# Performance work log

Measured on AMD Instinct MI355X. Metric: run time of the kernel, lower is better.

The kernel has to match this reference:

```python
import jax, jax.numpy as jnp
import numpy as np

B, C, H, W = 32, 16, 256, 256
NUM_BINS = 9
LEVELS = 3
EPS = 1e-8

def _dw_kernels():
    lap = np.array([[0, 1, 0], [1, -4, 1], [0, 1, 0]], np.float32)
    sx = np.array([[-1, 0, 1], [-2, 0, 2], [-1, 0, 1]], np.float32)
    sy = np.array([[-1, -2, -1], [0, 0, 0], [1, 2, 1]], np.float32)
    rep = lambda k: np.tile(k[None, None], (C, 1, 1, 1))  # [C,1,3,3] depthwise
    return rep(lap), rep(sx), rep(sy)

def setup_inputs() -> dict:
    key = jax.random.key(0)
    x = jax.random.normal(key, (B, C, H, W), dtype=jnp.float32)
    lap_k, sx_k, sy_k = _dw_kernels()
    return {"x": x, "lap_k": jnp.asarray(lap_k), "sx_k": jnp.asarray(sx_k), "sy_k": jnp.asarray(sy_k)}

def _dwconv(x, k):
    # depthwise 3x3, padding=1, groups=C
    return jax.lax.conv_general_dilated(
        x, k, window_strides=(1, 1), padding=[(1, 1), (1, 1)],
        dimension_numbers=("NCHW", "OIHW", "NCHW"), feature_group_count=C)

def reference(x, lap_k, sx_k, sy_k):
    lap = _dwconv(x, lap_k)
    gx = _dwconv(lap, sx_k)
    gy = _dwconv(lap, sy_k)
    mag = jnp.sqrt(gx * gx + gy * gy + EPS)
    ang = jnp.mod(jnp.arctan2(gy, gx) * (180.0 / np.pi), 180.0)
    bin_size = 180.0 / NUM_BINS
    bins = jnp.floor((ang + 0.5 * bin_size) / bin_size).astype(jnp.int32) % NUM_BINS

    BC = B * C
    mag_bc = mag.reshape(BC, H * W)
    bins_bc = bins.reshape(BC, H * W)
    row_ids = jnp.arange(BC)[:, None]

    hists = []
    for lvl in range(LEVELS):
        cs = 2 ** lvl
        cell_h, cell_w = H // cs, W // cs
        Wc = W // cell_w
        rows = jnp.arange(H) // cell_h
        cols = jnp.arange(W) // cell_w
        cell_id = (rows[:, None] * Wc + cols[None, :]).reshape(-1)  # [H*W]
        num_cells = cs * cs
        idx = cell_id[None, :] * NUM_BINS + bins_bc  # [BC, H*W]
        hist = jnp.zeros((BC, num_cells * NUM_BINS), mag.dtype).at[row_ids, idx].add(mag_bc)
        hist = hist.reshape(BC, num_cells, NUM_BINS)
        hist = hist / (hist.sum(axis=-1, keepdims=True) + EPS)          # L1-ish norm
        norm = jnp.sqrt(jnp.sum(hist * hist, axis=-1, keepdims=True))
        hist = hist / jnp.maximum(norm, 1e-12)                          # F.normalize p=2
        hists.append(hist.reshape(B, C * num_cells, NUM_BINS))
    out = jnp.concatenate(hists, axis=1)[:, None]  # [B,1,C*(1+4+16),num_bins]
    return out
```

## Files before the change

kernel.cpp:

```cpp
#include <hip/hip_runtime.h>


#define H_IMG 256
#define W_IMG 256

__device__ __forceinline__ void lap_row6(float dst[6], const float u[8], const float m[8],
                                         const float d[8], float wm0, float wm5, float rowm) {
#pragma unroll
  for (int c = 0; c < 6; ++c) {
    float v = (u[c + 1] + d[c + 1]) + fmaf(-4.f, m[c + 1], m[c] + m[c + 2]);
    dst[c] = v * rowm;
  }
  dst[0] *= wm0;
  dst[5] *= wm5;
}

__device__ __forceinline__ void out_row4(const float A[6], const float B[6], const float C[6],
                                         float acc[10]) {
  float cs[6], dd[6];
#pragma unroll
  for (int c = 0; c < 6; ++c) {
    cs[c] = A[c] + fmaf(2.f, B[c], C[c]);
    dd[c] = C[c] - A[c];
  }
#pragma unroll
  for (int c = 0; c < 4; ++c) {
    float gx = cs[c + 2] - cs[c];
    float gy = fmaf(2.f, dd[c + 1], dd[c] + dd[c + 2]);
    float mag = __builtin_amdgcn_sqrtf(fmaf(gx, gx, fmaf(gy, gy, 1e-8f)));
    bool neg = gy < 0.f;
    float fx = neg ? -gx : gx;
    float fy = neg ? -gy : gy;
    float u, v;
    u = 0.17364817766693033f * fx; v = 0.984807753012208f * fy;
    acc[0] += (u <= v) ? mag : 0.f;
    acc[8] += (u <= -v) ? mag : 0.f;
    u = 0.5f * fx; v = 0.8660254037844387f * fy;
    acc[1] += (u <= v) ? mag : 0.f;
    acc[7] += (u <= -v) ? mag : 0.f;
    u = 0.766044443118978f * fx; v = 0.6427876096865393f * fy;
    acc[2] += (u <= v) ? mag : 0.f;
    acc[6] += (u <= -v) ? mag : 0.f;
    u = 0.9396926207859084f * fx; v = 0.3420201433256687f * fy;
    acc[3] += (u <= v) ? mag : 0.f;
    acc[5] += (u <= -v) ? mag : 0.f;
    acc[4] += (fx <= 0.f) ? mag : 0.f;
    acc[9] += mag;
  }
}

__device__ __forceinline__ void load_grow(const float* __restrict__ xim, int gr, bool valid,
                                          int o0, int o1, int o2, int o3,
                                          float mlo, float mhi, float r[8]) {
  if (valid) {
    const float* p = xim + gr * W_IMG;
    float2 a = *reinterpret_cast<const float2*>(p + o0);
    float2 b = *reinterpret_cast<const float2*>(p + o1);
    float2 c = *reinterpret_cast<const float2*>(p + o2);
    float2 d = *reinterpret_cast<const float2*>(p + o3);
    r[0] = a.x * mlo; r[1] = a.y * mlo;
    r[2] = b.x;       r[3] = b.y;
    r[4] = c.x;       r[5] = c.y;
    r[6] = d.x * mhi; r[7] = d.y * mhi;
  } else {
#pragma unroll
    for (int i = 0; i < 8; ++i) r[i] = 0.f;
  }
}

__global__ __launch_bounds__(256) void phog_hist_kernel(const float* __restrict__ x,
                                                        float* __restrict__ hist2) {
  const int f = blockIdx.y * 16 + blockIdx.x;
  const int xcd = f & 7;
  const int idx = f >> 3;
  const int bc = xcd * 64 + (idx >> 4);
  const int tile = idx & 15;
  const int R0 = (tile >> 2) * 64;
  const int C0 = (tile & 3) * 64;
  const int tid = threadIdx.x;
  const int tcol = tid & 15;
  const int trow = tid >> 4;

  const float* xim = x + (size_t)bc * (H_IMG * W_IMG);

  const int gr0 = R0 + 4 * trow;
  const int gc0 = C0 + 4 * tcol;
  const int bcol = gc0 - 2;

  const int o0 = (bcol < 0) ? 0 : bcol;
  const int o1 = gc0;
  const int o2 = gc0 + 2;
  const int o3 = (gc0 + 4 > 254) ? 254 : (gc0 + 4);
  const float mlo = (bcol >= 0) ? 1.f : 0.f;
  const float mhi = (gc0 + 5 <= 255) ? 1.f : 0.f;

  const bool vlo = gr0 > 0;
  const bool vhi = gr0 < 252;
  const float rm_first = vlo ? 1.f : 0.f;
  const float rm_last = (gr0 + 4 <= 255) ? 1.f : 0.f;
  const float wm0 = (gc0 >= 1) ? 1.f : 0.f;
  const float wm5 = (gc0 + 4 <= 255) ? 1.f : 0.f;

  float w0[8], w1[8], w2[8], w3[8], w4[8], w5[8], w6[8], w7[8];
  load_grow(xim, gr0 - 2, vlo, o0, o1, o2, o3, mlo, mhi, w0);
  load_grow(xim, gr0 - 1, vlo, o0, o1, o2, o3, mlo, mhi, w1);
  load_grow(xim, gr0 + 0, true, o0, o1, o2, o3, mlo, mhi, w2);
  load_grow(xim, gr0 + 1, true, o0, o1, o2, o3, mlo, mhi, w3);
  load_grow(xim, gr0 + 2, true, o0, o1, o2, o3, mlo, mhi, w4);
  load_grow(xim, gr0 + 3, true, o0, o1, o2, o3, mlo, mhi, w5);
  load_grow(xim, gr0 + 4, vhi, o0, o1, o2, o3, mlo, mhi, w6);
  load_grow(xim, gr0 + 5, vhi, o0, o1, o2, o3, mlo, mhi, w7);

  float acc[10];
#pragma unroll
  for (int k = 0; k < 10; ++k) acc[k] = 0.f;

  float lA[6], lB[6], lC[6], lD[6];
  lap_row6(lA, w0, w1, w2, wm0, wm5, rm_first);
  lap_row6(lB, w1, w2, w3, wm0, wm5, 1.f);
  lap_row6(lC, w2, w3, w4, wm0, wm5, 1.f);
  out_row4(lA, lB, lC, acc);
  lap_row6(lD, w3, w4, w5, wm0, wm5, 1.f);
  out_row4(lB, lC, lD, acc);
  lap_row6(lA, w4, w5, w6, wm0, wm5, 1.f);
  out_row4(lC, lD, lA, acc);
  lap_row6(lB, w5, w6, w7, wm0, wm5, rm_last);
  out_row4(lD, lA, lB, acc);

#pragma unroll
  for (int k = 0; k < 10; ++k) {
    float v = acc[k];
#pragma unroll
    for (int off = 32; off > 0; off >>= 1) v += __shfl_xor(v, off);
    acc[k] = v;
  }

  __shared__ float hred[4][10];
  __shared__ float hsum[10];
  const int lane = tid & 63;
  const int wave = tid >> 6;
  if (lane == 0) {
#pragma unroll
    for (int k = 0; k < 10; ++k) hred[wave][k] = acc[k];
  }
  __syncthreads();
  if (tid < 10) hsum[tid] = (hred[0][tid] + hred[1][tid]) + (hred[2][tid] + hred[3][tid]);
  __syncthreads();
  if (tid < 9) {
    float h = (tid == 0) ? ((hsum[9] - hsum[0]) + hsum[8]) : (hsum[tid - 1] - hsum[tid]);
    hist2[(bc * 16 + tile) * 9 + tid] = h;
  }
}

__global__ __launch_bounds__(256) void phog_norm_kernel(const float* __restrict__ hist2,
                                                        float* __restrict__ out) {
  int t = blockIdx.x * 256 + threadIdx.x;
  if (t >= 32 * 336) return;
  int b = t / 336;
  int r = t - b * 336;

  float h[9];
  if (r < 16) {
    const float* p = hist2 + (b * 16 + r) * 144;
#pragma unroll
    for (int k = 0; k < 9; ++k) {
      float s = 0.f;
#pragma unroll
      for (int cell = 0; cell < 16; ++cell) s += p[cell * 9 + k];
      h[k] = s;
    }
  } else if (r < 80) {
    int q = r - 16;
    int c = q >> 2;
    int cell = q & 3;
    int r1 = cell >> 1, c1 = cell & 1;
    const float* p = hist2 + (b * 16 + c) * 144;
    int i00 = ((2 * r1) * 4 + 2 * c1) * 9;
    int i01 = ((2 * r1) * 4 + 2 * c1 + 1) * 9;
    int i10 = ((2 * r1 + 1) * 4 + 2 * c1) * 9;
    int i11 = ((2 * r1 + 1) * 4 + 2 * c1 + 1) * 9;
#pragma unroll
    for (int k = 0; k < 9; ++k) h[k] = (p[i00 + k] + p[i01 + k]) + (p[i10 + k] + p[i11 + k]);
  } else {
    int q = r - 80;
    int c = q >> 4;
    int cell = q & 15;
    const float* p = hist2 + ((b * 16 + c) * 16 + cell) * 9;
#pragma unroll
    for (int k = 0; k < 9; ++k) h[k] = p[k];
  }

  float s = 0.f;
#pragma unroll
  for (int k = 0; k < 9; ++k) s += h[k];
  float inv = 1.f / (s + 1e-8f);
#pragma unroll
  for (int k = 0; k < 9; ++k) h[k] *= inv;
  float n2 = 0.f;
#pragma unroll
  for (int k = 0; k < 9; ++k) n2 = fmaf(h[k], h[k], n2);
  float nrm = sqrtf(n2);
  float inv2 = 1.f / fmaxf(nrm, 1e-12f);
#pragma unroll
  for (int k = 0; k < 9; ++k) out[t * 9 + k] = h[k] * inv2;
}

extern "C" void kernel_launch(void* const* d_in, const int* in_sizes, int n_in,
                              void* d_out, int out_size, void* d_ws, size_t ws_size,
                              hipStream_t stream) {
  const float* x = (const float*)d_in[0];
  float* out = (float*)d_out;
  float* hist2 = (float*)d_ws;

  dim3 g1(16, 512);
  phog_hist_kernel<<<g1, 256, 0, stream>>>(x, hist2);

  int total = 32 * 336;
  phog_norm_kernel<<<(total + 255) / 256, 256, 0, stream>>>(hist2, out);
}
```

Measured before the change: 64.97 us.

## Enlarge per-thread tile to 8x8 with rolling rows and branchless binning

Each thread now computes an 8x8 output patch using a rolling three-row register window, which lowers the halo overhead per output pixel. The grid drops to 4 column tiles per image, and each wave covers one 64x64 cell, so the shared-memory reduction and block barriers go away. Bin comparisons are replaced by scaled fmed3 clamps fused into FMA accumulation, with the goal of removing selects. The clamp relies on huge scale constants acting as a step function, so results differ slightly from exact comparisons when values sit near bin boundaries. The XCD-aware block swizzle is dropped, and each thread now holds more registers.

```diff
diff --git a/kernel.cpp b/kernel.cpp
--- a/kernel.cpp
+++ b/kernel.cpp
@@ -4,128 +4,142 @@
 #define H_IMG 256
 #define W_IMG 256
 
-__device__ __forceinline__ void lap_row6(float dst[6], const float u[8], const float m[8],
-                                         const float d[8], float wm0, float wm5, float rowm) {
-#pragma unroll
-  for (int c = 0; c < 6; ++c) {
-    float v = (u[c + 1] + d[c + 1]) + fmaf(-4.f, m[c + 1], m[c] + m[c + 2]);
-    dst[c] = v * rowm;
+#define S0 1.7364817766693033e34f
+#define C0 9.84807753012208e34f
+#define S1 5.0e34f
+#define C1 8.660254037844387e34f
+#define S2 7.66044443118978e34f
+#define C2 6.427876096865393e34f
+#define S3 9.396926207859084e34f
+#define C3 3.420201433256687e34f
+
+__device__ __forceinline__ void load_xrow12(const float* __restrict__ xim, int gr, bool valid,
+                                            int o0, int o5, int gc0, float mlo, float mhi,
+                                            float r[12]) {
+  if (valid) {
+    const float* p = xim + gr * W_IMG;
+    float2 a = *reinterpret_cast<const float2*>(p + o0);
+    float2 b = *reinterpret_cast<const float2*>(p + gc0);
+    float2 c = *reinterpret_cast<const float2*>(p + gc0 + 2);
+    float2 d = *reinterpret_cast<const float2*>(p + gc0 + 4);
+    float2 e = *reinterpret_cast<const float2*>(p + gc0 + 6);
+    float2 f = *reinterpret_cast<const float2*>(p + o5);
+    r[0] = a.x * mlo; r[1] = a.y * mlo;
+    r[2] = b.x;  r[3] = b.y;  r[4] = c.x;  r[5] = c.y;
+    r[6] = d.x;  r[7] = d.y;  r[8] = e.x;  r[9] = e.y;
+    r[10] = f.x * mhi; r[11] = f.y * mhi;
+  } else {
+#pragma unroll
+    for (int i = 0; i < 12; ++i) r[i] = 0.f;
+  }
+}
+
+__device__ __forceinline__ void lap_row10(float dst[10], const float u[12], const float m[12],
+                                          const float d[12], float wm0, float wm9, float rowm) {
+#pragma unroll
+  for (int j = 0; j < 10; ++j) {
+    float v = (u[j + 1] + d[j + 1]) + fmaf(-4.f, m[j + 1], m[j] + m[j + 2]);
+    dst[j] = v * rowm;
   }
   dst[0] *= wm0;
-  dst[5] *= wm5;
-}
-
-__device__ __forceinline__ void out_row4(const float A[6], const float B[6], const float C[6],
+  dst[9] *= wm9;
+}
+
+__device__ __forceinline__ void out_row8(const float A[10], const float B[10], const float C[10],
                                          float acc[10]) {
-  float cs[6], dd[6];
-#pragma unroll
-  for (int c = 0; c < 6; ++c) {
-    cs[c] = A[c] + fmaf(2.f, B[c], C[c]);
-    dd[c] = C[c] - A[c];
-  }
-#pragma unroll
-  for (int c = 0; c < 4; ++c) {
+  float cs[10], dd[10];
+#pragma unroll
+  for (int j = 0; j < 10; ++j) {
+    cs[j] = A[j] + fmaf(2.f, B[j], C[j]);
+    dd[j] = C[j] - A[j];
+  }
+#pragma unroll
+  for (int c = 0; c < 8; ++c) {
     float gx = cs[c + 2] - cs[c];
     float gy = fmaf(2.f, dd[c + 1], dd[c] + dd[c + 2]);
     float mag = __builtin_amdgcn_sqrtf(fmaf(gx, gx, fmaf(gy, gy, 1e-8f)));
-    bool neg = gy < 0.f;
-    float fx = neg ? -gx : gx;
-    float fy = neg ? -gy : gy;
-    float u, v;
-    u = 0.17364817766693033f * fx; v = 0.984807753012208f * fy;
-    acc[0] += (u <= v) ? mag : 0.f;
-    acc[8] += (u <= -v) ? mag : 0.f;
-    u = 0.5f * fx; v = 0.8660254037844387f * fy;
-    acc[1] += (u <= v) ? mag : 0.f;
-    acc[7] += (u <= -v) ? mag : 0.f;
-    u = 0.766044443118978f * fx; v = 0.6427876096865393f * fy;
-    acc[2] += (u <= v) ? mag : 0.f;
-    acc[6] += (u <= -v) ? mag : 0.f;
-    u = 0.9396926207859084f * fx; v = 0.3420201433256687f * fy;
-    acc[3] += (u <= v) ? mag : 0.f;
-    acc[5] += (u <= -v) ? mag : 0.f;
-    acc[4] += (fx <= 0.f) ? mag : 0.f;
+    unsigned sg = __float_as_uint(gy) & 0x80000000u;
+    float fx = __uint_as_float(__float_as_uint(gx) ^ sg);
+    float fy = fabsf(gy);
+    float b0 = fx * S0;
+    acc[0] = fmaf(mag, __builtin_amdgcn_fmed3f(fmaf(fy, C0, -b0), 0.f, 1.f), acc[0]);
+    acc[8] = fmaf(mag, __builtin_amdgcn_fmed3f(fmaf(fy, -C0, -b0), 0.f, 1.f), acc[8]);
+    float b1 = fx * S1;
+    acc[1] = fmaf(mag, __builtin_amdgcn_fmed3f(fmaf(fy, C1, -b1), 0.f, 1.f), acc[1]);
+    acc[7] = fmaf(mag, __builtin_amdgcn_fmed3f(fmaf(fy, -C1, -b1), 0.f, 1.f), acc[7]);
+    float b2 = fx * S2;
+    acc[2] = fmaf(mag, __builtin_amdgcn_fmed3f(fmaf(fy, C2, -b2), 0.f, 1.f), acc[2]);
+    acc[6] = fmaf(mag, __builtin_amdgcn_fmed3f(fmaf(fy, -C2, -b2), 0.f, 1.f), acc[6]);
+    float b3 = fx * S3;
+    acc[3] = fmaf(mag, __builtin_amdgcn_fmed3f(fmaf(fy, C3, -b3), 0.f, 1.f), acc[3]);
+    acc[5] = fmaf(mag, __builtin_amdgcn_fmed3f(fmaf(fy, -C3, -b3), 0.f, 1.f), acc[5]);
+    acc[4] = fmaf(mag, __builtin_amdgcn_fmed3f(fx * -1e35f, 0.f, 1.f), acc[4]);
     acc[9] += mag;
-  }
-}
-
-__device__ __forceinline__ void load_grow(const float* __restrict__ xim, int gr, bool valid,
-                                          int o0, int o1, int o2, int o3,
-                                          float mlo, float mhi, float r[8]) {
-  if (valid) {
-    const float* p = xim + gr * W_IMG;
-    float2 a = *reinterpret_cast<const float2*>(p + o0);
-    float2 b = *reinterpret_cast<const float2*>(p + o1);
-    float2 c = *reinterpret_cast<const float2*>(p + o2);
-    float2 d = *reinterpret_cast<const float2*>(p + o3);
-    r[0] = a.x * mlo; r[1] = a.y * mlo;
-    r[2] = b.x;       r[3] = b.y;
-    r[4] = c.x;       r[5] = c.y;
-    r[6] = d.x * mhi; r[7] = d.y * mhi;
-  } else {
-#pragma unroll
-    for (int i = 0; i < 8; ++i) r[i] = 0.f;
   }
 }
 
 __global__ __launch_bounds__(256) void phog_hist_kernel(const float* __restrict__ x,
                                                         float* __restrict__ hist2) {
-  const int f = blockIdx.y * 16 + blockIdx.x;
-  const int xcd = f & 7;
-  const int idx = f >> 3;
-  const int bc = xcd * 64 + (idx >> 4);
-  const int tile = idx & 15;
-  const int R0 = (tile >> 2) * 64;
-  const int C0 = (tile & 3) * 64;
+  const int tc = blockIdx.x;
+  const int bc = blockIdx.y;
   const int tid = threadIdx.x;
-  const int tcol = tid & 15;
-  const int trow = tid >> 4;
+  const int tcol = tid & 7;
+  const int trow = tid >> 3;
 
   const float* xim = x + (size_t)bc * (H_IMG * W_IMG);
 
-  const int gr0 = R0 + 4 * trow;
-  const int gc0 = C0 + 4 * tcol;
-  const int bcol = gc0 - 2;
-
-  const int o0 = (bcol < 0) ? 0 : bcol;
-  const int o1 = gc0;
-  const int o2 = gc0 + 2;
-  const int o3 = (gc0 + 4 > 254) ? 254 : (gc0 + 4);
-  const float mlo = (bcol >= 0) ? 1.f : 0.f;
-  const float mhi = (gc0 + 5 <= 255) ? 1.f : 0.f;
-
-  const bool vlo = gr0 > 0;
-  const bool vhi = gr0 < 252;
-  const float rm_first = vlo ? 1.f : 0.f;
-  const float rm_last = (gr0 + 4 <= 255) ? 1.f : 0.f;
+  const int gr0 = 8 * trow;
+  const int gc0 = tc * 64 + 8 * tcol;
+
+  const int o0 = (gc0 - 2 < 0) ? 0 : (gc0 - 2);
+  const int o5 = (gc0 + 8 > 254) ? 254 : (gc0 + 8);
+  const float mlo = (gc0 - 2 >= 0) ? 1.f : 0.f;
+  const float mhi = (gc0 + 9 <= 255) ? 1.f : 0.f;
   const float wm0 = (gc0 >= 1) ? 1.f : 0.f;
-  const float wm5 = (gc0 + 4 <= 255) ? 1.f : 0.f;
-
-  float w0[8], w1[8], w2[8], w3[8], w4[8], w5[8], w6[8], w7[8];
-  load_grow(xim, gr0 - 2, vlo, o0, o1, o2, o3, mlo, mhi, w0);
-  load_grow(xim, gr0 - 1, vlo, o0, o1, o2, o3, mlo, mhi, w1);
-  load_grow(xim, gr0 + 0, true, o0, o1, o2, o3, mlo, mhi, w2);
-  load_grow(xim, gr0 + 1, true, o0, o1, o2, o3, mlo, mhi, w3);
-  load_grow(xim, gr0 + 2, true, o0, o1, o2, o3, mlo, mhi, w4);
-  load_grow(xim, gr0 + 3, true, o0, o1, o2, o3, mlo, mhi, w5);
-  load_grow(xim, gr0 + 4, vhi, o0, o1, o2, o3, mlo, mhi, w6);
-  load_grow(xim, gr0 + 5, vhi, o0, o1, o2, o3, mlo, mhi, w7);
+  const float wm9 = (gc0 + 8 <= 255) ? 1.f : 0.f;
+
+  const bool vlo = trow > 0;
+  const bool vhi = trow < 31;
+  const float rmf = vlo ? 1.f : 0.f;
+  const float rml = vhi ? 1.f : 0.f;
 
   float acc[10];
 #pragma unroll
   for (int k = 0; k < 10; ++k) acc[k] = 0.f;
 
-  float lA[6], lB[6], lC[6], lD[6];
-  lap_row6(lA, w0, w1, w2, wm0, wm5, rm_first);
-  lap_row6(lB, w1, w2, w3, wm0, wm5, 1.f);
-  lap_row6(lC, w2, w3, w4, wm0, wm5, 1.f);
-  out_row4(lA, lB, lC, acc);
-  lap_row6(lD, w3, w4, w5, wm0, wm5, 1.f);
-  out_row4(lB, lC, lD, acc);
-  lap_row6(lA, w4, w5, w6, wm0, wm5, 1.f);
-  out_row4(lC, lD, lA, acc);
-  lap_row6(lB, w5, w6, w7, wm0, wm5, rm_last);
-  out_row4(lD, lA, lB, acc);
+  float xa[12], xb[12], xc[12];
+  float La[10], Lb[10], Lc[10];
+
+  load_xrow12(xim, gr0 - 2, vlo, o0, o5, gc0, mlo, mhi, xa);
+  load_xrow12(xim, gr0 - 1, vlo, o0, o5, gc0, mlo, mhi, xb);
+  load_xrow12(xim, gr0 + 0, true, o0, o5, gc0, mlo, mhi, xc);
+  lap_row10(La, xa, xb, xc, wm0, wm9, rmf);
+  load_xrow12(xim, gr0 + 1, true, o0, o5, gc0, mlo, mhi, xa);
+  lap_row10(Lb, xb, xc, xa, wm0, wm9, 1.f);
+  load_xrow12(xim, gr0 + 2, true, o0, o5, gc0, mlo, mhi, xb);
+  lap_row10(Lc, xc, xa, xb, wm0, wm9, 1.f);
+  out_row8(La, Lb, Lc, acc);
+  load_xrow12(xim, gr0 + 3, true, o0, o5, gc0, mlo, mhi, xc);
+  lap_row10(La, xa, xb, xc, wm0, wm9, 1.f);
+  out_row8(Lb, Lc, La, acc);
+  load_xrow12(xim, gr0 + 4, true, o0, o5, gc0, mlo, mhi, xa);
+  lap_row10(Lb, xb, xc, xa, wm0, wm9, 1.f);
+  out_row8(Lc, La, Lb, acc);
+  load_xrow12(xim, gr0 + 5, true, o0, o5, gc0, mlo, mhi, xb);
+  lap_row10(Lc, xc, xa, xb, wm0, wm9, 1.f);
+  out_row8(La, Lb, Lc, acc);
+  load_xrow12(xim, gr0 + 6, true, o0, o5, gc0, mlo, mhi, xc);
+  lap_row10(La, xa, xb, xc, wm0, wm9, 1.f);
+  out_row8(Lb, Lc, La, acc);
+  load_xrow12(xim, gr0 + 7, true, o0, o5, gc0, mlo, mhi, xa);
+  lap_row10(Lb, xb, xc, xa, wm0, wm9, 1.f);
+  out_row8(Lc, La, Lb, acc);
+  load_xrow12(xim, gr0 + 8, vhi, o0, o5, gc0, mlo, mhi, xb);
+  lap_row10(Lc, xc, xa, xb, wm0, wm9, 1.f);
+  out_row8(La, Lb, Lc, acc);
+  load_xrow12(xim, gr0 + 9, vhi, o0, o5, gc0, mlo, mhi, xc);
+  lap_row10(La, xa, xb, xc, wm0, wm9, rml);
+  out_row8(Lb, Lc, La, acc);
 
 #pragma unroll
   for (int k = 0; k < 10; ++k) {
@@ -134,21 +148,13 @@
     for (int off = 32; off > 0; off >>= 1) v += __shfl_xor(v, off);
     acc[k] = v;
   }
-
-  __shared__ float hred[4][10];
-  __shared__ float hsum[10];
   const int lane = tid & 63;
-  const int wave = tid >> 6;
+  const int w = tid >> 6;
   if (lane == 0) {
-#pragma unroll
-    for (int k = 0; k < 10; ++k) hred[wave][k] = acc[k];
-  }
-  __syncthreads();
-  if (tid < 10) hsum[tid] = (hred[0][tid] + hred[1][tid]) + (hred[2][tid] + hred[3][tid]);
-  __syncthreads();
-  if (tid < 9) {
-    float h = (tid == 0) ? ((hsum[9] - hsum[0]) + hsum[8]) : (hsum[tid - 1] - hsum[tid]);
-    hist2[(bc * 16 + tile) * 9 + tid] = h;
+    float* dst = &hist2[((bc * 16) + (w * 4 + tc)) * 9];
+    dst[0] = (acc[9] - acc[0]) + acc[8];
+#pragma unroll
+    for (int k = 1; k < 9; ++k) dst[k] = acc[k - 1] - acc[k];
   }
 }
 
@@ -212,7 +218,7 @@
   float* out = (float*)d_out;
   float* hist2 = (float*)d_ws;
 
-  dim3 g1(16, 512);
+  dim3 g1(4, 512);
   phog_hist_kernel<<<g1, 256, 0, stream>>>(x, hist2);
 
   int total = 32 * 336;
```

Result: faster. 62.94 us (-3.1%).
